# Performance work log

Measured on AMD Instinct MI355X. Metric: run time of the kernel, lower is better.

The kernel has to match this reference:

```python
import jax, jax.numpy as jnp
import numpy as np

B, T, E = 2, 2048, 2048
H, H_KV, D = 16, 8, 128
THETA = 10000.0


def setup_inputs() -> dict:
    key = jax.random.key(0)
    ks = jax.random.split(key, 5)
    s = lambda n: (1.0 / np.sqrt(n))
    x = jax.random.normal(ks[0], (B, T, E), dtype=jnp.float32)
    wq = jax.random.normal(ks[1], (E, H * D), dtype=jnp.float32) * s(E)
    wk = jax.random.normal(ks[2], (E, H_KV * D), dtype=jnp.float32) * s(E)
    wv = jax.random.normal(ks[3], (E, H_KV * D), dtype=jnp.float32) * s(E)
    wo = jax.random.normal(ks[4], (H * D, E), dtype=jnp.float32) * s(H * D)
    # causal mask, broadcast over batch and heads
    mask = jnp.tril(jnp.ones((T, T), dtype=jnp.int32))[None, None, :, :]
    return {"x": x, "mask": mask, "wq": wq, "wk": wk, "wv": wv, "wo": wo}


def _rope(q, k):
    # q,k: [B,H,T,D]; deinterleave even/odd, rotate, concat halves (as in source)
    Tq, Dh = q.shape[2], q.shape[3] // 2
    inv = 1.0 / (THETA ** (jnp.arange(Dh, dtype=jnp.float32) / Dh))
    ang = jnp.arange(Tq, dtype=jnp.float32)[:, None] * inv[None, :]  # [T,Dh]
    c, s = jnp.cos(ang), jnp.sin(ang)  # broadcast over [B,H]
    q1, q2 = q[..., ::2], q[..., 1::2]
    k1, k2 = k[..., ::2], k[..., 1::2]
    q_rot = jnp.concatenate([q1 * c - q2 * s, q2 * c + q1 * s], axis=-1)
    k_rot = jnp.concatenate([k1 * c - k2 * s, k2 * c + k1 * s], axis=-1)
    return q_rot, k_rot


def reference(x, mask, wq, wk, wv, wo):
    Bx, Tx, _ = x.shape
    scale = D ** -0.5
    q = (x @ wq).reshape(Bx, Tx, H, D).transpose(0, 2, 1, 3)      # [B,H,T,D]
    k = (x @ wk).reshape(Bx, Tx, H_KV, D).transpose(0, 2, 1, 3)   # [B,Hkv,T,D]
    v = (x @ wv).reshape(Bx, Tx, H_KV, D).transpose(0, 2, 1, 3)
    # torch .repeat tiles along head axis: [kv0..kv7, kv0..kv7]
    k = jnp.tile(k, (1, H // H_KV, 1, 1))
    v = jnp.tile(v, (1, H // H_KV, 1, 1))
    q, k = _rope(q, k)
    attn = jnp.einsum('bhtd,bhsd->bhts', q, k) * scale
    attn = jnp.where(mask == 0, -jnp.inf, attn)
    w = jax.nn.softmax(attn, axis=-1)
    w = jnp.where(jnp.isnan(w), 0.0, w)
    out = jnp.einsum('bhts,bhsd->bhtd', w, v)
    out = out.transpose(0, 2, 1, 3).reshape(Bx, Tx, H * D)
    return out @ wo
```

## Files before the change

### kernel.cpp

```cpp
#include <hip/hip_runtime.h>
#include <hip/hip_bf16.h>
#include <cstdint>

typedef short bf16x8 __attribute__((ext_vector_type(8)));
typedef float f32x4 __attribute__((ext_vector_type(4)));
typedef unsigned short u16;
typedef unsigned int u32;

#define TT 2048

__device__ __forceinline__ u16 f2bf(float f) {
    __hip_bfloat16 h = __float2bfloat16(f);
    return __builtin_bit_cast(u16, h);
}
__device__ __forceinline__ float bf2f(u16 u) {
    return __builtin_bit_cast(float, (u32)u << 16);
}
__device__ __forceinline__ f32x4 mfma16(bf16x8 a, bf16x8 b, f32x4 c) {
    return __builtin_amdgcn_mfma_f32_16x16x32_bf16(a, b, c, 0, 0, 0);
}
__device__ __forceinline__ bf16x8 ldg8(const u16* p) {
    return __builtin_bit_cast(bf16x8, *reinterpret_cast<const uint4*>(p));
}
__device__ __forceinline__ bf16x8 lds8(const u16* p) {
    return *reinterpret_cast<const bf16x8*>(p);
}
__device__ __forceinline__ void gll16(const u16* g, u16* l) {
    __builtin_amdgcn_global_load_lds(
        (const __attribute__((address_space(1))) void*)g,
        (__attribute__((address_space(3))) void*)l, 16, 0, 0);
}

__global__ __launch_bounds__(256) void cast_f32_bf16(const float* __restrict__ src,
                                                     u16* __restrict__ dst, int n) {
    int idx = (blockIdx.x * 256 + threadIdx.x) * 8;
    if (idx + 7 >= n + 8) return;
    float4 a = *reinterpret_cast<const float4*>(&src[idx]);
    float4 b = *reinterpret_cast<const float4*>(&src[idx + 4]);
    u16 o[8] = {f2bf(a.x), f2bf(a.y), f2bf(a.z), f2bf(a.w),
                f2bf(b.x), f2bf(b.y), f2bf(b.z), f2bf(b.w)};
    *reinterpret_cast<uint4*>(&dst[idx]) = *reinterpret_cast<const uint4*>(o);
}

template <int ROPE>
__global__ __launch_bounds__(256) void transpose_cast(const float* __restrict__ src,
                                                      u16* __restrict__ dst, int R, int C) {
    __shared__ float tl[64][65];
    const int tid = threadIdx.x;
    const int cb = blockIdx.x, rb = blockIdx.y;
#pragma unroll
    for (int i = 0; i < 16; i++) {
        int li = i * 256 + tid;
        int tr = li >> 6, tc = li & 63;
        tl[tr][tc] = src[(size_t)(rb * 64 + tr) * C + cb * 64 + tc];
    }
    __syncthreads();
#pragma unroll
    for (int i = 0; i < 16; i++) {
        int li = i * 256 + tid;
        int dr = li >> 6, dc = li & 63;
        int c = cb * 64 + dr;
        int j;
        if (ROPE) {
            int head = c >> 7, cl = c & 127, ii = cl >> 1, odd = cl & 1;
            j = head * 128 + ((ii & 15) | (odd << 4) | ((ii >> 4) << 5));
        } else {
            j = c;
        }
        dst[(size_t)j * R + rb * 64 + dc] = f2bf(tl[dc][dr]);
    }
}

template <int MODE>
__global__ __launch_bounds__(256) void gemm_bt(const u16* __restrict__ A,
                                               const u16* __restrict__ BT,
                                               void* __restrict__ P0, void* __restrict__ P1,
                                               void* __restrict__ P2, int M, int N, int K) {
    __shared__ __align__(16) u16 smA[2][128 * 64];
    __shared__ __align__(16) u16 smB[2][128 * 64];
    const int tid = threadIdx.x;
    const int w = tid >> 6, lane = tid & 63, quad = lane >> 4, l15 = lane & 15;
    const int wr = w >> 1, wc = w & 1;
    const int bm = blockIdx.y, bn = blockIdx.x;

    f32x4 acc[4][4];
    const f32x4 zf = {0.f, 0.f, 0.f, 0.f};
#pragma unroll
    for (int i = 0; i < 4; i++)
#pragma unroll
        for (int j = 0; j < 4; j++) acc[i][j] = zf;

    const u16* aSrc[4];
    const u16* bSrc[4];
#pragma unroll
    for (int i = 0; i < 4; i++) {
        int o = i * 256 + w * 64 + lane;
        int r = o >> 3, p = o & 7;
        int cc = p ^ (r & 7);
        aSrc[i] = A + (size_t)(bm * 128 + r) * K + cc * 8;
        bSrc[i] = BT + (size_t)(bn * 128 + r) * K + cc * 8;
    }
    auto stage = [&](int buf) {
#pragma unroll
        for (int i = 0; i < 4; i++) {
            gll16(aSrc[i], &smA[buf][(i * 256 + w * 64) * 8]);
            gll16(bSrc[i], &smB[buf][(i * 256 + w * 64) * 8]);
            aSrc[i] += 64;
            bSrc[i] += 64;
        }
    };

    stage(0);
    const int nkt = K >> 6;
    for (int kt = 0; kt < nkt; ++kt) {
        const int cur = kt & 1;
        __syncthreads();
        if (kt + 1 < nkt) stage(cur ^ 1);
#pragma unroll
        for (int ks = 0; ks < 2; ++ks) {
            const int cd = ks * 4 + quad;
            bf16x8 af[4], bf[4];
#pragma unroll
            for (int mi = 0; mi < 4; mi++) {
                int row = wr * 64 + mi * 16 + l15;
                af[mi] = lds8(&smA[cur][row * 64 + (cd ^ (row & 7)) * 8]);
            }
#pragma unroll
            for (int ni = 0; ni < 4; ni++) {
                int row = wc * 64 + ni * 16 + l15;
                bf[ni] = lds8(&smB[cur][row * 64 + (cd ^ (row & 7)) * 8]);
            }
#pragma unroll
            for (int mi = 0; mi < 4; mi++)
#pragma unroll
                for (int ni = 0; ni < 4; ni++) acc[mi][ni] = mfma16(af[mi], bf[ni], acc[mi][ni]);
        }
    }

    if (MODE == 1) {
#pragma unroll
        for (int mi = 0; mi < 4; mi++)
#pragma unroll
            for (int ni = 0; ni < 4; ni++)
#pragma unroll
                for (int r = 0; r < 4; r++) {
                    int m = bm * 128 + wr * 64 + mi * 16 + quad * 4 + r;
                    int n = bn * 128 + wc * 64 + ni * 16 + l15;
                    ((float*)P0)[(size_t)m * N + n] = acc[mi][ni][r];
                }
    } else if (bn < 24) {
#pragma unroll
        for (int mi = 0; mi < 4; mi++)
#pragma unroll
            for (int g = 0; g < 2; g++) {
                int i = (wc * 2 + g) * 16 + l15;
                float inv = __expf(-0.14391156644f * (float)i);
#pragma unroll
                for (int r = 0; r < 4; r++) {
                    int m = bm * 128 + wr * 64 + mi * 16 + quad * 4 + r;
                    int b = m >> 11, t = m & 2047;
                    float ang = (float)t * inv;
                    float sn, cs;
                    __sincosf(ang, &sn, &cs);
                    float x1 = acc[mi][2 * g][r], x2 = acc[mi][2 * g + 1][r];
                    u16 o1 = f2bf(x1 * cs - x2 * sn);
                    u16 o2 = f2bf(x2 * cs + x1 * sn);
                    if (bn < 16) {
                        u16* pq = (u16*)P0 + ((size_t)(b * 16 + bn) * 2048 + t) * 128;
                        pq[i] = o1;
                        pq[i + 64] = o2;
                    } else {
                        u16* pk = (u16*)P1 + ((size_t)(b * 8 + (bn - 16)) * 2048 + t) * 128;
                        pk[i] = o1;
                        pk[i + 64] = o2;
                    }
                }
            }
    } else {
#pragma unroll
        for (int mi = 0; mi < 4; mi++)
#pragma unroll
            for (int ni = 0; ni < 4; ni++)
#pragma unroll
                for (int r = 0; r < 4; r++) {
                    int m = bm * 128 + wr * 64 + mi * 16 + quad * 4 + r;
                    int b = m >> 11, t = m & 2047;
                    int d = wc * 64 + ni * 16 + l15;
                    int h = bn - 24;
                    ((u16*)P2)[((size_t)(b * 8 + h) * 128 + d) * 2048 + t] =
                        f2bf(acc[mi][ni][r]);
                }
    }
}

__global__ __launch_bounds__(256) void flash_attn(const u16* __restrict__ qg,
                                                  const u16* __restrict__ kg,
                                                  const u16* __restrict__ vg,
                                                  u16* __restrict__ og) {
    __shared__ __align__(16) u16 Ksm[2][64 * 128];
    __shared__ __align__(16) u16 Vsm[2][128 * 64];
    __shared__ __align__(16) u16 Pt[4 * 32 * 72];
    const int tid = threadIdx.x, w = tid >> 6, lane = tid & 63, quad = lane >> 4,
              l15 = lane & 15;
    const int bkv = blockIdx.x;
    const int qblk = 31 - (int)blockIdx.y;
    const int b = bkv >> 3, kvh = bkv & 7;
    const float scale = 0.08838834764831845f;

    const u16* kb = kg + (size_t)(b * 8 + kvh) * 2048 * 128;
    const u16* vb = vg + (size_t)(b * 8 + kvh) * 128 * 2048;

    bf16x8 aq[2][4];
#pragma unroll
    for (int hh = 0; hh < 2; hh++) {
        const int h = kvh + hh * 8;
        const u16* qp =
            qg + ((size_t)(b * 16 + h) * 2048 + qblk * 64 + w * 16 + l15) * 128 + quad * 8;
#pragma unroll
        for (int kk = 0; kk < 4; kk++) aq[hh][kk] = ldg8(qp + kk * 32);
    }

    f32x4 oacc[2][8];
    f32x4 lacc[2];
    const f32x4 zf = {0.f, 0.f, 0.f, 0.f};
#pragma unroll
    for (int hh = 0; hh < 2; hh++) {
        lacc[hh] = zf;
#pragma unroll
        for (int j = 0; j < 8; j++) oacc[hh][j] = zf;
    }
    bf16x8 ones;
#pragma unroll
    for (int i = 0; i < 8; i++) ones[i] = (short)0x3F80;

    auto stage = [&](int st, int buf) {
#pragma unroll
        for (int i = 0; i < 4; i++) {
            int o = i * 256 + w * 64 + lane;
            int s = o >> 4, p = o & 15;
            int cc = (p & 8) | ((p ^ s) & 7);
            gll16(kb + (size_t)(st * 64 + s) * 128 + cc * 8, &Ksm[buf][(i * 256 + w * 64) * 8]);
            int d = o >> 3, p2 = o & 7;
            int cc2 = (p2 ^ d) & 7;
            gll16(vb + (size_t)d * 2048 + st * 64 + cc2 * 8, &Vsm[buf][(i * 256 + w * 64) * 8]);
        }
    };

    stage(0, 0);
    for (int st = 0; st <= qblk; ++st) {
        const int cur = st & 1;
        __syncthreads();
        if (st < qblk) stage(st + 1, cur ^ 1);

        f32x4 s0[4], s1[4];
#pragma unroll
        for (int j = 0; j < 4; j++) {
            s0[j] = zf;
            s1[j] = zf;
#pragma unroll
            for (int kk = 0; kk < 4; kk++) {
                int srow = j * 16 + l15;
                int cd = kk * 4 + quad;
                int p = (cd & 8) | ((cd ^ srow) & 7);
                bf16x8 bk = lds8(&Ksm[cur][srow * 128 + p * 8]);
                s0[j] = mfma16(aq[0][kk], bk, s0[j]);
                s1[j] = mfma16(aq[1][kk], bk, s1[j]);
            }
        }
        const bool diag = (st == qblk);
#pragma unroll
        for (int j = 0; j < 4; j++)
#pragma unroll
            for (int r = 0; r < 4; r++) {
                bool masked = diag && (j * 16 + l15) > (w * 16 + quad * 4 + r);
                float p0 = masked ? 0.f : __expf(s0[j][r] * scale);
                float p1 = masked ? 0.f : __expf(s1[j][r] * scale);
                int prow = w * 32 + quad * 4 + r;
                Pt[prow * 72 + j * 16 + l15] = f2bf(p0);
                Pt[(prow + 16) * 72 + j * 16 + l15] = f2bf(p1);
            }
#pragma unroll
        for (int kk = 0; kk < 2; kk++) {
            bf16x8 ap0 = lds8(&Pt[(w * 32 + l15) * 72 + kk * 32 + quad * 8]);
            bf16x8 ap1 = lds8(&Pt[(w * 32 + 16 + l15) * 72 + kk * 32 + quad * 8]);
#pragma unroll
            for (int jf = 0; jf < 8; jf++) {
                int drow = jf * 16 + l15;
                int cd2 = kk * 4 + quad;
                int p2 = (cd2 ^ drow) & 7;
                bf16x8 bv = lds8(&Vsm[cur][drow * 64 + p2 * 8]);
                oacc[0][jf] = mfma16(ap0, bv, oacc[0][jf]);
                oacc[1][jf] = mfma16(ap1, bv, oacc[1][jf]);
            }
            lacc[0] = mfma16(ap0, ones, lacc[0]);
            lacc[1] = mfma16(ap1, ones, lacc[1]);
        }
    }
#pragma unroll
    for (int hh = 0; hh < 2; hh++) {
        const int h = kvh + hh * 8;
#pragma unroll
        for (int jf = 0; jf < 8; jf++)
#pragma unroll
            for (int r = 0; r < 4; r++) {
                int t = qblk * 64 + w * 16 + quad * 4 + r;
                int d = jf * 16 + l15;
                og[((size_t)(b * 2048 + t) * 16 + h) * 128 + d] =
                    f2bf(oacc[hh][jf][r] / lacc[hh][r]);
            }
    }
}

extern "C" void kernel_launch(void* const* d_in, const int* in_sizes, int n_in, void* d_out,
                              int out_size, void* d_ws, size_t ws_size, hipStream_t stream) {
    const float* x = (const float*)d_in[0];
    const float* wq = (const float*)d_in[2];
    const float* wk = (const float*)d_in[3];
    const float* wv = (const float*)d_in[4];
    const float* wo = (const float*)d_in[5];
    float* out = (float*)d_out;

    char* ws = (char*)d_ws;
    u16* xb = (u16*)(ws);
    u16* wqkvT = (u16*)(ws + 16777216);
    u16* woT = (u16*)(ws + 33554432);
    u16* qbuf = (u16*)(ws + 41943040);
    u16* kbuf = (u16*)(ws + 58720256);
    u16* vtb = (u16*)(ws + 67108864);
    u16* obuf = xb;

    cast_f32_bf16<<<4096, 256, 0, stream>>>(x, xb, 8388608);
    transpose_cast<1><<<dim3(32, 32), 256, 0, stream>>>(wq, wqkvT, 2048, 2048);
    transpose_cast<1><<<dim3(16, 32), 256, 0, stream>>>(wk, wqkvT + 2048 * 2048, 2048, 1024);
    transpose_cast<0><<<dim3(16, 32), 256, 0, stream>>>(wv, wqkvT + 3072 * 2048, 2048, 1024);
    transpose_cast<0><<<dim3(32, 32), 256, 0, stream>>>(wo, woT, 2048, 2048);

    gemm_bt<0><<<dim3(32, 32), 256, 0, stream>>>(xb, wqkvT, qbuf, kbuf, vtb, 4096, 4096, 2048);

    flash_attn<<<dim3(16, 32), 256, 0, stream>>>(qbuf, kbuf, vtb, obuf);

    gemm_bt<1><<<dim3(16, 32), 256, 0, stream>>>(obuf, woT, out, nullptr, nullptr, 4096, 2048,
                                                 2048);
}
```

Baseline: 325.8 us.

## Load B/K/V operands directly from global into registers, drop LDS staging

```diff
diff --git a/kernel.cpp b/kernel.cpp
--- a/kernel.cpp
+++ b/kernel.cpp
@@ -72,12 +72,11 @@
 }
 
 template <int MODE>
-__global__ __launch_bounds__(256) void gemm_bt(const u16* __restrict__ A,
-                                               const u16* __restrict__ BT,
-                                               void* __restrict__ P0, void* __restrict__ P1,
-                                               void* __restrict__ P2, int M, int N, int K) {
+__global__ __launch_bounds__(256, 2) void gemm_bt(const u16* __restrict__ A,
+                                                  const u16* __restrict__ BT,
+                                                  void* __restrict__ P0, void* __restrict__ P1,
+                                                  void* __restrict__ P2, int M, int N, int K) {
     __shared__ __align__(16) u16 smA[2][128 * 64];
-    __shared__ __align__(16) u16 smB[2][128 * 64];
     const int tid = threadIdx.x;
     const int w = tid >> 6, lane = tid & 63, quad = lane >> 4, l15 = lane & 15;
     const int wr = w >> 1, wc = w & 1;
@@ -91,50 +90,67 @@
         for (int j = 0; j < 4; j++) acc[i][j] = zf;
 
     const u16* aSrc[4];
-    const u16* bSrc[4];
 #pragma unroll
     for (int i = 0; i < 4; i++) {
-        int o = i * 256 + w * 64 + lane;
+        int o = i * 256 + tid;
         int r = o >> 3, p = o & 7;
         int cc = p ^ (r & 7);
         aSrc[i] = A + (size_t)(bm * 128 + r) * K + cc * 8;
-        bSrc[i] = BT + (size_t)(bn * 128 + r) * K + cc * 8;
-    }
-    auto stage = [&](int buf) {
+    }
+    auto stageA = [&](int buf) {
 #pragma unroll
         for (int i = 0; i < 4; i++) {
             gll16(aSrc[i], &smA[buf][(i * 256 + w * 64) * 8]);
-            gll16(bSrc[i], &smB[buf][(i * 256 + w * 64) * 8]);
             aSrc[i] += 64;
-            bSrc[i] += 64;
         }
     };
 
-    stage(0);
-    const int nkt = K >> 6;
-    for (int kt = 0; kt < nkt; ++kt) {
-        const int cur = kt & 1;
-        __syncthreads();
-        if (kt + 1 < nkt) stage(cur ^ 1);
+    const u16* bBase[4];
+#pragma unroll
+    for (int ni = 0; ni < 4; ni++)
+        bBase[ni] = BT + (size_t)(bn * 128 + wc * 64 + ni * 16 + l15) * K + quad * 8;
+    auto loadB = [&](bf16x8* d, int koff) {
+#pragma unroll
+        for (int ni = 0; ni < 4; ni++) {
+            d[ni * 2] = ldg8(bBase[ni] + koff);
+            d[ni * 2 + 1] = ldg8(bBase[ni] + koff + 32);
+        }
+    };
+    auto compute = [&](int abuf, const bf16x8* b) {
 #pragma unroll
         for (int ks = 0; ks < 2; ++ks) {
             const int cd = ks * 4 + quad;
-            bf16x8 af[4], bf[4];
+            bf16x8 af[4];
 #pragma unroll
             for (int mi = 0; mi < 4; mi++) {
                 int row = wr * 64 + mi * 16 + l15;
-                af[mi] = lds8(&smA[cur][row * 64 + (cd ^ (row & 7)) * 8]);
-            }
-#pragma unroll
-            for (int ni = 0; ni < 4; ni++) {
-                int row = wc * 64 + ni * 16 + l15;
-                bf[ni] = lds8(&smB[cur][row * 64 + (cd ^ (row & 7)) * 8]);
+                af[mi] = lds8(&smA[abuf][row * 64 + (cd ^ (row & 7)) * 8]);
             }
 #pragma unroll
             for (int mi = 0; mi < 4; mi++)
 #pragma unroll
-                for (int ni = 0; ni < 4; ni++) acc[mi][ni] = mfma16(af[mi], bf[ni], acc[mi][ni]);
-        }
+                for (int ni = 0; ni < 4; ni++)
+                    acc[mi][ni] = mfma16(af[mi], b[ni * 2 + ks], acc[mi][ni]);
+        }
+    };
+
+    bf16x8 bA[8], bB[8];
+    loadB(bA, 0);
+    stageA(0);
+    const int nkt = K >> 6;
+    for (int kt = 0; kt < nkt; kt += 2) {
+        __syncthreads();
+        if (kt + 1 < nkt) {
+            stageA(1);
+            loadB(bB, (kt + 1) * 64);
+        }
+        compute(0, bA);
+        __syncthreads();
+        if (kt + 2 < nkt) {
+            stageA(0);
+            loadB(bA, (kt + 2) * 64);
+        }
+        compute(1, bB);
     }
 
     if (MODE == 1) {
@@ -193,12 +209,10 @@
     }
 }
 
-__global__ __launch_bounds__(256) void flash_attn(const u16* __restrict__ qg,
-                                                  const u16* __restrict__ kg,
-                                                  const u16* __restrict__ vg,
-                                                  u16* __restrict__ og) {
-    __shared__ __align__(16) u16 Ksm[2][64 * 128];
-    __shared__ __align__(16) u16 Vsm[2][128 * 64];
+__global__ __launch_bounds__(256, 2) void flash_attn(const u16* __restrict__ qg,
+                                                     const u16* __restrict__ kg,
+                                                     const u16* __restrict__ vg,
+                                                     u16* __restrict__ og) {
     __shared__ __align__(16) u16 Pt[4 * 32 * 72];
     const int tid = threadIdx.x, w = tid >> 6, lane = tid & 63, quad = lane >> 4,
               l15 = lane & 15;
@@ -233,24 +247,17 @@
 #pragma unroll
     for (int i = 0; i < 8; i++) ones[i] = (short)0x3F80;
 
-    auto stage = [&](int st, int buf) {
-#pragma unroll
-        for (int i = 0; i < 4; i++) {
-            int o = i * 256 + w * 64 + lane;
-            int s = o >> 4, p = o & 15;
-            int cc = (p & 8) | ((p ^ s) & 7);
-            gll16(kb + (size_t)(st * 64 + s) * 128 + cc * 8, &Ksm[buf][(i * 256 + w * 64) * 8]);
-            int d = o >> 3, p2 = o & 7;
-            int cc2 = (p2 ^ d) & 7;
-            gll16(vb + (size_t)d * 2048 + st * 64 + cc2 * 8, &Vsm[buf][(i * 256 + w * 64) * 8]);
-        }
-    };
-
-    stage(0, 0);
+    const u16* kB[4];
+#pragma unroll
+    for (int j = 0; j < 4; j++) kB[j] = kb + (size_t)(j * 16 + l15) * 128 + quad * 8;
+    const u16* vB[8];
+#pragma unroll
+    for (int jf = 0; jf < 8; jf++) vB[jf] = vb + (size_t)(jf * 16 + l15) * 2048 + quad * 8;
+
     for (int st = 0; st <= qblk; ++st) {
-        const int cur = st & 1;
-        __syncthreads();
-        if (st < qblk) stage(st + 1, cur ^ 1);
+        bf16x8 vf0[8], vf1[8];
+#pragma unroll
+        for (int jf = 0; jf < 8; jf++) vf0[jf] = ldg8(vB[jf]);
 
         f32x4 s0[4], s1[4];
 #pragma unroll
@@ -259,14 +266,14 @@
             s1[j] = zf;
 #pragma unroll
             for (int kk = 0; kk < 4; kk++) {
-                int srow = j * 16 + l15;
-                int cd = kk * 4 + quad;
-                int p = (cd & 8) | ((cd ^ srow) & 7);
-                bf16x8 bk = lds8(&Ksm[cur][srow * 128 + p * 8]);
+                bf16x8 bk = ldg8(kB[j] + kk * 32);
                 s0[j] = mfma16(aq[0][kk], bk, s0[j]);
                 s1[j] = mfma16(aq[1][kk], bk, s1[j]);
             }
         }
+#pragma unroll
+        for (int jf = 0; jf < 8; jf++) vf1[jf] = ldg8(vB[jf] + 32);
+
         const bool diag = (st == qblk);
 #pragma unroll
         for (int j = 0; j < 4; j++)
@@ -285,16 +292,17 @@
             bf16x8 ap1 = lds8(&Pt[(w * 32 + 16 + l15) * 72 + kk * 32 + quad * 8]);
 #pragma unroll
             for (int jf = 0; jf < 8; jf++) {
-                int drow = jf * 16 + l15;
-                int cd2 = kk * 4 + quad;
-                int p2 = (cd2 ^ drow) & 7;
-                bf16x8 bv = lds8(&Vsm[cur][drow * 64 + p2 * 8]);
+                bf16x8 bv = kk ? vf1[jf] : vf0[jf];
                 oacc[0][jf] = mfma16(ap0, bv, oacc[0][jf]);
                 oacc[1][jf] = mfma16(ap1, bv, oacc[1][jf]);
             }
             lacc[0] = mfma16(ap0, ones, lacc[0]);
             lacc[1] = mfma16(ap1, ones, lacc[1]);
         }
+#pragma unroll
+        for (int j = 0; j < 4; j++) kB[j] += 64 * 128;
+#pragma unroll
+        for (int jf = 0; jf < 8; jf++) vB[jf] += 64;
     }
 #pragma unroll
     for (int hh = 0; hh < 2; hh++) {
```

Result: slower. 533.8 us (+63.8%).

## Halve GEMM K-tile to raise occupancy and merge weight transpose launches

Applied to the files above, without the earlier changes.

```diff
diff --git a/kernel.cpp b/kernel.cpp
--- a/kernel.cpp
+++ b/kernel.cpp
@@ -42,12 +42,26 @@
     *reinterpret_cast<uint4*>(&dst[idx]) = *reinterpret_cast<const uint4*>(o);
 }
 
-template <int ROPE>
-__global__ __launch_bounds__(256) void transpose_cast(const float* __restrict__ src,
-                                                      u16* __restrict__ dst, int R, int C) {
+__global__ __launch_bounds__(256) void transpose_cast_all(const float* __restrict__ wq,
+                                                          const float* __restrict__ wk,
+                                                          const float* __restrict__ wv,
+                                                          const float* __restrict__ wo,
+                                                          u16* __restrict__ wqkvT,
+                                                          u16* __restrict__ woT) {
+    const int z = blockIdx.z;
+    const float* src;
+    u16* dst;
+    int C, rope;
+    const int R = 2048;
+    if (z == 0) { src = wq; dst = wqkvT;               C = 2048; rope = 1; }
+    else if (z == 1) { src = wk; dst = wqkvT + 2048 * 2048; C = 1024; rope = 1; }
+    else if (z == 2) { src = wv; dst = wqkvT + 3072 * 2048; C = 1024; rope = 0; }
+    else { src = wo; dst = woT;                        C = 2048; rope = 0; }
+    const int cb = blockIdx.x, rb = blockIdx.y;
+    if (cb * 64 >= C) return;
+
     __shared__ float tl[64][65];
     const int tid = threadIdx.x;
-    const int cb = blockIdx.x, rb = blockIdx.y;
 #pragma unroll
     for (int i = 0; i < 16; i++) {
         int li = i * 256 + tid;
@@ -61,7 +75,7 @@
         int dr = li >> 6, dc = li & 63;
         int c = cb * 64 + dr;
         int j;
-        if (ROPE) {
+        if (rope) {
             int head = c >> 7, cl = c & 127, ii = cl >> 1, odd = cl & 1;
             j = head * 128 + ((ii & 15) | (odd << 4) | ((ii >> 4) << 5));
         } else {
@@ -72,12 +86,12 @@
 }
 
 template <int MODE>
-__global__ __launch_bounds__(256) void gemm_bt(const u16* __restrict__ A,
-                                               const u16* __restrict__ BT,
-                                               void* __restrict__ P0, void* __restrict__ P1,
-                                               void* __restrict__ P2, int M, int N, int K) {
-    __shared__ __align__(16) u16 smA[2][128 * 64];
-    __shared__ __align__(16) u16 smB[2][128 * 64];
+__global__ __launch_bounds__(256, 4) void gemm_bt(const u16* __restrict__ A,
+                                                  const u16* __restrict__ BT,
+                                                  void* __restrict__ P0, void* __restrict__ P1,
+                                                  void* __restrict__ P2, int M, int N, int K) {
+    __shared__ __align__(16) u16 smA[2][128 * 32];
+    __shared__ __align__(16) u16 smB[2][128 * 32];
     const int tid = threadIdx.x;
     const int w = tid >> 6, lane = tid & 63, quad = lane >> 4, l15 = lane & 15;
     const int wr = w >> 1, wc = w & 1;
@@ -90,51 +104,47 @@
 #pragma unroll
         for (int j = 0; j < 4; j++) acc[i][j] = zf;
 
-    const u16* aSrc[4];
-    const u16* bSrc[4];
-#pragma unroll
-    for (int i = 0; i < 4; i++) {
-        int o = i * 256 + w * 64 + lane;
-        int r = o >> 3, p = o & 7;
-        int cc = p ^ (r & 7);
+    const u16* aSrc[2];
+    const u16* bSrc[2];
+#pragma unroll
+    for (int i = 0; i < 2; i++) {
+        int o = i * 256 + tid;
+        int r = o >> 2, p = o & 3;
+        int cc = p ^ ((r >> 1) & 3);
         aSrc[i] = A + (size_t)(bm * 128 + r) * K + cc * 8;
         bSrc[i] = BT + (size_t)(bn * 128 + r) * K + cc * 8;
     }
     auto stage = [&](int buf) {
 #pragma unroll
-        for (int i = 0; i < 4; i++) {
+        for (int i = 0; i < 2; i++) {
             gll16(aSrc[i], &smA[buf][(i * 256 + w * 64) * 8]);
             gll16(bSrc[i], &smB[buf][(i * 256 + w * 64) * 8]);
-            aSrc[i] += 64;
-            bSrc[i] += 64;
+            aSrc[i] += 32;
+            bSrc[i] += 32;
         }
     };
 
     stage(0);
-    const int nkt = K >> 6;
+    const int nkt = K >> 5;
     for (int kt = 0; kt < nkt; ++kt) {
         const int cur = kt & 1;
         __syncthreads();
         if (kt + 1 < nkt) stage(cur ^ 1);
-#pragma unroll
-        for (int ks = 0; ks < 2; ++ks) {
-            const int cd = ks * 4 + quad;
-            bf16x8 af[4], bf[4];
-#pragma unroll
-            for (int mi = 0; mi < 4; mi++) {
-                int row = wr * 64 + mi * 16 + l15;
-                af[mi] = lds8(&smA[cur][row * 64 + (cd ^ (row & 7)) * 8]);
-            }
-#pragma unroll
-            for (int ni = 0; ni < 4; ni++) {
-                int row = wc * 64 + ni * 16 + l15;
-                bf[ni] = lds8(&smB[cur][row * 64 + (cd ^ (row & 7)) * 8]);
-            }
-#pragma unroll
-            for (int mi = 0; mi < 4; mi++)
-#pragma unroll
-                for (int ni = 0; ni < 4; ni++) acc[mi][ni] = mfma16(af[mi], bf[ni], acc[mi][ni]);
-        }
+        bf16x8 af[4], bf[4];
+#pragma unroll
+        for (int mi = 0; mi < 4; mi++) {
+            int row = wr * 64 + mi * 16 + l15;
+            af[mi] = lds8(&smA[cur][row * 32 + (quad ^ ((row >> 1) & 3)) * 8]);
+        }
+#pragma unroll
+        for (int ni = 0; ni < 4; ni++) {
+            int row = wc * 64 + ni * 16 + l15;
+            bf[ni] = lds8(&smB[cur][row * 32 + (quad ^ ((row >> 1) & 3)) * 8]);
+        }
+#pragma unroll
+        for (int mi = 0; mi < 4; mi++)
+#pragma unroll
+            for (int ni = 0; ni < 4; ni++) acc[mi][ni] = mfma16(af[mi], bf[ni], acc[mi][ni]);
     }
 
     if (MODE == 1) {
@@ -330,10 +340,7 @@
     u16* obuf = xb;
 
     cast_f32_bf16<<<4096, 256, 0, stream>>>(x, xb, 8388608);
-    transpose_cast<1><<<dim3(32, 32), 256, 0, stream>>>(wq, wqkvT, 2048, 2048);
-    transpose_cast<1><<<dim3(16, 32), 256, 0, stream>>>(wk, wqkvT + 2048 * 2048, 2048, 1024);
-    transpose_cast<0><<<dim3(16, 32), 256, 0, stream>>>(wv, wqkvT + 3072 * 2048, 2048, 1024);
-    transpose_cast<0><<<dim3(32, 32), 256, 0, stream>>>(wo, woT, 2048, 2048);
+    transpose_cast_all<<<dim3(32, 32, 4), 256, 0, stream>>>(wq, wk, wv, wo, wqkvT, woT);
 
     gemm_bt<0><<<dim3(32, 32), 256, 0, stream>>>(xb, wqkvT, qbuf, kbuf, vtb, 4096, 4096, 2048);
 
```

New measurement: 338.1 us. +3.8%, slower.

## Merge prologue cast/transpose kernels into one launch and XOR-swizzle P tile

Applied to the files above, without the earlier changes.

```diff
diff --git a/kernel.cpp b/kernel.cpp
--- a/kernel.cpp
+++ b/kernel.cpp
@@ -31,23 +31,41 @@
         (__attribute__((address_space(3))) void*)l, 16, 0, 0);
 }
 
-__global__ __launch_bounds__(256) void cast_f32_bf16(const float* __restrict__ src,
-                                                     u16* __restrict__ dst, int n) {
-    int idx = (blockIdx.x * 256 + threadIdx.x) * 8;
-    if (idx + 7 >= n + 8) return;
-    float4 a = *reinterpret_cast<const float4*>(&src[idx]);
-    float4 b = *reinterpret_cast<const float4*>(&src[idx + 4]);
-    u16 o[8] = {f2bf(a.x), f2bf(a.y), f2bf(a.z), f2bf(a.w),
-                f2bf(b.x), f2bf(b.y), f2bf(b.z), f2bf(b.w)};
-    *reinterpret_cast<uint4*>(&dst[idx]) = *reinterpret_cast<const uint4*>(o);
-}
-
-template <int ROPE>
-__global__ __launch_bounds__(256) void transpose_cast(const float* __restrict__ src,
-                                                      u16* __restrict__ dst, int R, int C) {
+__global__ __launch_bounds__(256) void prologue(const float* __restrict__ x,
+                                                const float* __restrict__ wq,
+                                                const float* __restrict__ wk,
+                                                const float* __restrict__ wv,
+                                                const float* __restrict__ wo,
+                                                u16* __restrict__ xb,
+                                                u16* __restrict__ wqkvT,
+                                                u16* __restrict__ woT) {
+    const int z = blockIdx.z;
+    const int tid = threadIdx.x;
+    if (z == 4) {
+        int bix = blockIdx.y * 32 + blockIdx.x;
+#pragma unroll
+        for (int k = 0; k < 4; k++) {
+            int idx = (bix * 1024 + k * 256 + tid) * 8;
+            float4 a = *reinterpret_cast<const float4*>(&x[idx]);
+            float4 b = *reinterpret_cast<const float4*>(&x[idx + 4]);
+            u16 o[8] = {f2bf(a.x), f2bf(a.y), f2bf(a.z), f2bf(a.w),
+                        f2bf(b.x), f2bf(b.y), f2bf(b.z), f2bf(b.w)};
+            *reinterpret_cast<uint4*>(&xb[idx]) = *reinterpret_cast<const uint4*>(o);
+        }
+        return;
+    }
+    const float* src;
+    u16* dst;
+    int C, rope;
+    const int R = 2048;
+    if (z == 0) { src = wq; dst = wqkvT;               C = 2048; rope = 1; }
+    else if (z == 1) { src = wk; dst = wqkvT + 2048 * 2048; C = 1024; rope = 1; }
+    else if (z == 2) { src = wv; dst = wqkvT + 3072 * 2048; C = 1024; rope = 0; }
+    else { src = wo; dst = woT;                        C = 2048; rope = 0; }
+    const int cb = blockIdx.x, rb = blockIdx.y;
+    if (cb * 64 >= C) return;
+
     __shared__ float tl[64][65];
-    const int tid = threadIdx.x;
-    const int cb = blockIdx.x, rb = blockIdx.y;
 #pragma unroll
     for (int i = 0; i < 16; i++) {
         int li = i * 256 + tid;
@@ -61,7 +79,7 @@
         int dr = li >> 6, dc = li & 63;
         int c = cb * 64 + dr;
         int j;
-        if (ROPE) {
+        if (rope) {
             int head = c >> 7, cl = c & 127, ii = cl >> 1, odd = cl & 1;
             j = head * 128 + ((ii & 15) | (odd << 4) | ((ii >> 4) << 5));
         } else {
@@ -94,7 +112,7 @@
     const u16* bSrc[4];
 #pragma unroll
     for (int i = 0; i < 4; i++) {
-        int o = i * 256 + w * 64 + lane;
+        int o = i * 256 + tid;
         int r = o >> 3, p = o & 7;
         int cc = p ^ (r & 7);
         aSrc[i] = A + (size_t)(bm * 128 + r) * K + cc * 8;
@@ -199,7 +217,7 @@
                                                   u16* __restrict__ og) {
     __shared__ __align__(16) u16 Ksm[2][64 * 128];
     __shared__ __align__(16) u16 Vsm[2][128 * 64];
-    __shared__ __align__(16) u16 Pt[4 * 32 * 72];
+    __shared__ __align__(16) u16 Pt[4 * 32 * 64];
     const int tid = threadIdx.x, w = tid >> 6, lane = tid & 63, quad = lane >> 4,
               l15 = lane & 15;
     const int bkv = blockIdx.x;
@@ -276,17 +294,21 @@
                 float p0 = masked ? 0.f : __expf(s0[j][r] * scale);
                 float p1 = masked ? 0.f : __expf(s1[j][r] * scale);
                 int prow = w * 32 + quad * 4 + r;
-                Pt[prow * 72 + j * 16 + l15] = f2bf(p0);
-                Pt[(prow + 16) * 72 + j * 16 + l15] = f2bf(p1);
+                int cc = (j * 2 + (l15 >> 3));
+                int off = (l15 & 7);
+                Pt[prow * 64 + ((cc ^ (prow & 7)) * 8) + off] = f2bf(p0);
+                int prow1 = prow + 16;
+                Pt[prow1 * 64 + ((cc ^ (prow1 & 7)) * 8) + off] = f2bf(p1);
             }
 #pragma unroll
         for (int kk = 0; kk < 2; kk++) {
-            bf16x8 ap0 = lds8(&Pt[(w * 32 + l15) * 72 + kk * 32 + quad * 8]);
-            bf16x8 ap1 = lds8(&Pt[(w * 32 + 16 + l15) * 72 + kk * 32 + quad * 8]);
+            int row0 = w * 32 + l15, row1 = row0 + 16;
+            int cd2 = kk * 4 + quad;
+            bf16x8 ap0 = lds8(&Pt[row0 * 64 + ((cd2 ^ (row0 & 7)) * 8)]);
+            bf16x8 ap1 = lds8(&Pt[row1 * 64 + ((cd2 ^ (row1 & 7)) * 8)]);
 #pragma unroll
             for (int jf = 0; jf < 8; jf++) {
                 int drow = jf * 16 + l15;
-                int cd2 = kk * 4 + quad;
                 int p2 = (cd2 ^ drow) & 7;
                 bf16x8 bv = lds8(&Vsm[cur][drow * 64 + p2 * 8]);
                 oacc[0][jf] = mfma16(ap0, bv, oacc[0][jf]);
@@ -329,11 +351,7 @@
     u16* vtb = (u16*)(ws + 67108864);
     u16* obuf = xb;
 
-    cast_f32_bf16<<<4096, 256, 0, stream>>>(x, xb, 8388608);
-    transpose_cast<1><<<dim3(32, 32), 256, 0, stream>>>(wq, wqkvT, 2048, 2048);
-    transpose_cast<1><<<dim3(16, 32), 256, 0, stream>>>(wk, wqkvT + 2048 * 2048, 2048, 1024);
-    transpose_cast<0><<<dim3(16, 32), 256, 0, stream>>>(wv, wqkvT + 3072 * 2048, 2048, 1024);
-    transpose_cast<0><<<dim3(32, 32), 256, 0, stream>>>(wo, woT, 2048, 2048);
+    prologue<<<dim3(32, 32, 5), 256, 0, stream>>>(x, wq, wk, wv, wo, xb, wqkvT, woT);
 
     gemm_bt<0><<<dim3(32, 32), 256, 0, stream>>>(xb, wqkvT, qbuf, kbuf, vtb, 4096, 4096, 2048);
 
```

Result: faster. 312.5 us (-4.1%).
